# Kernel optimization log

Hardware: AMD Instinct MI355X
Metric: run time of the kernel (lower is better)

## Reference

```python
import jax, jax.numpy as jnp
import numpy as np

N_HEADS = 8
WINDOW = 7

def _conv1x1(x, W, b):
    # x: [B,H,W,C]; 1x1 conv == per-pixel matmul
    return jnp.einsum('bhwc,cd->bhwd', x, W) + b

def _to_heads(t, nh):
    # [B,H,W,C] -> channels-first reshape [B, nh, C//nh, H*W] (matches tf transpose+reshape)
    B, H, W, C = t.shape
    return jnp.transpose(t, (0, 3, 1, 2)).reshape(B, nh, C // nh, H * W)

def setup_inputs() -> dict:
    key = jax.random.key(0)
    ks = jax.random.split(key, 8)
    B, H, W, C = 2, 56, 56, 256
    x = jax.random.normal(ks[0], (B, H, W, C), dtype=jnp.float32)
    s = 1.0 / np.sqrt(C)
    Wq = jax.random.normal(ks[1], (C, C), dtype=jnp.float32) * s
    bq = jnp.zeros((C,), dtype=jnp.float32)
    Wk = jax.random.normal(ks[2], (C, C), dtype=jnp.float32) * s
    bk = jnp.zeros((C,), dtype=jnp.float32)
    Wv = jax.random.normal(ks[3], (C, C), dtype=jnp.float32) * s
    bv = jnp.zeros((C,), dtype=jnp.float32)
    # original initializes gamma to 0 (output == x); use small nonzero so the
    # attention path is observable in outputs/grads
    gamma = jax.random.normal(ks[4], (1,), dtype=jnp.float32) * 0.1
    return {"x": x, "Wq": Wq, "bq": bq, "Wk": Wk, "bk": bk, "Wv": Wv, "bv": bv, "gamma": gamma}

def reference(x, Wq, bq, Wk, bk, Wv, bv, gamma):
    B, H, W, C = x.shape
    p = WINDOW // 2
    xp = jnp.pad(x, ((0, 0), (p, p), (p, p), (0, 0)), mode='reflect')  # [B,Hp,Wp,C]
    q = _to_heads(_conv1x1(x, Wq, bq), N_HEADS)    # [B,nh,dk,HW]
    k = _to_heads(_conv1x1(xp, Wk, bk), N_HEADS)   # [B,nh,dk,HpWp]
    v = _to_heads(_conv1x1(xp, Wv, bv), N_HEADS)   # [B,nh,dk,HpWp]
    energy = jnp.einsum('bhdq,bhdk->bhqk', q, k)   # [B,nh,HW,HpWp]
    attn = jax.nn.softmax(energy, axis=-1)
    out = jnp.einsum('bhdk,bhqk->bhdq', v, attn)   # [B,nh,dk,HW]
    out = out.reshape(B, C, H, W).transpose(0, 2, 3, 1)
    return gamma * out + x
```

## Files before the change

### kernel.cpp

```cpp
#include <hip/hip_runtime.h>

typedef unsigned short u16;
typedef float f32x4 __attribute__((ext_vector_type(4)));
typedef short bf16x8 __attribute__((ext_vector_type(8)));

__device__ __forceinline__ u16 f2bf(float f) {
    unsigned u = __float_as_uint(f);
    u = (u + 0x7FFFu + ((u >> 16) & 1u)) >> 16;
    return (u16)u;
}

#define LOG2E 1.4426950408889634f

#if __has_builtin(__builtin_amdgcn_exp2f)
__device__ __forceinline__ float exp2_fast(float x) { return __builtin_amdgcn_exp2f(x); }
#else
__device__ __forceinline__ float exp2_fast(float x) { return __expf(x * 0.6931471805599453f); }
#endif

__device__ __forceinline__ unsigned pack2bf(float a, float b) {
    unsigned ua = __float_as_uint(a) + 0x8000u;
    unsigned ub = __float_as_uint(b) + 0x8000u;
#if __has_builtin(__builtin_amdgcn_perm)
    return __builtin_amdgcn_perm(ub, ua, 0x07060302u);
#else
    return ((ua >> 16) & 0xFFFFu) | (ub & 0xFFFF0000u);
#endif
}

#if __has_builtin(__builtin_amdgcn_cvt_pk_bf16_f32)
typedef __bf16 bf2_t __attribute__((ext_vector_type(2)));
__device__ __forceinline__ unsigned cvtpk(float a, float b) {
    bf2_t r = __builtin_amdgcn_cvt_pk_bf16_f32(a, b);
    return __builtin_bit_cast(unsigned, r);
}
#else
__device__ __forceinline__ unsigned cvtpk(float a, float b) { return pack2bf(a, b); }
#endif

__device__ __forceinline__ bf16x8 bc8(uint4 u) { return __builtin_bit_cast(bf16x8, u); }

#if __has_builtin(__builtin_amdgcn_global_load_lds)
typedef const __attribute__((address_space(1))) void* as1cv;
typedef __attribute__((address_space(3))) void* as3v;
__device__ __forceinline__ void dma16(const void* g, void* lds_base, int lane) {
    __builtin_amdgcn_global_load_lds((as1cv)g, (as3v)lds_base, 16, 0, 0);
}
#else
__device__ __forceinline__ void dma16(const void* g, void* lds_base, int lane) {
    *(uint4*)((char*)lds_base + lane * 16) = *(const uint4*)g;
}
#endif

#define BB 2
#define HH 56
#define SQ 3136
#define SKP 3200
#define VT_STRIDE 3200
#define CROWN 3584

#define WS_Q    0
#define WS_K    1605632
#define WS_VT   3211264
#define WS_WT   4849664
#define WS_CB   5046272

__global__ __launch_bounds__(256) void wprep_kernel(const float* __restrict__ Wq,
                                                    const float* __restrict__ Wk,
                                                    const float* __restrict__ Wv,
                                                    u16* __restrict__ wtf,
                                                    u16* __restrict__ vtb,
                                                    u16* __restrict__ crow) {
    __shared__ u16 T[64][68];
    int mode = blockIdx.z;
    const float* W = (mode == 0) ? Wq : ((mode == 1) ? Wk : Wv);
    float sc = (mode == 0) ? LOG2E : 1.0f;
    int kx = blockIdx.x * 64, dx = blockIdx.y * 64;
    int tid = threadIdx.x;
    int r16 = tid >> 4, c4 = (tid & 15) * 4;
#pragma unroll
    for (int p = 0; p < 4; ++p) {
        int kr = p * 16 + r16;
        float4 f = *(const float4*)&W[(size_t)(kx + kr) * 256 + dx + c4];
        T[kr][c4 + 0] = f2bf(f.x * sc);
        T[kr][c4 + 1] = f2bf(f.y * sc);
        T[kr][c4 + 2] = f2bf(f.z * sc);
        T[kr][c4 + 3] = f2bf(f.w * sc);
    }
    __syncthreads();
    int l16 = tid & 15, nt_loc = (tid >> 4) & 3, quad = (tid >> 6) & 3;
#pragma unroll
    for (int s_loc = 0; s_loc < 2; ++s_loc) {
        int k0 = s_loc * 32 + quad * 8;
        int d_loc = nt_loc * 16 + l16;
        u16 tmp[8];
#pragma unroll
        for (int j = 0; j < 8; ++j) tmp[j] = T[k0 + j][d_loc];
        int d = dx + d_loc;
        int nz = d >> 7, ntg = (d >> 4) & 7;
        int s = (kx >> 5) + s_loc;
        int f = (nz * 8 + s) * 8 + ntg;
        int L = quad * 16 + l16;
        *(uint4*)&wtf[(size_t)mode * 65536 + (size_t)f * 512 + (size_t)L * 8] = *(uint4*)tmp;
    }
    if (mode == 1 && kx == 0 && dx == 0) {
        for (int i = tid; i < CROWN; i += 256) {
            u16 v = 0;
            if (i < SQ) {
                int rr = i / 56, cc = i - rr * 56;
                int mr = (((rr >= 1) && (rr <= 3)) || ((rr >= 52) && (rr <= 54))) ? 2 : 1;
                int mc = (((cc >= 1) && (cc <= 3)) || ((cc >= 52) && (cc <= 54))) ? 2 : 1;
                int prod = mr * mc;
                v = (prod == 1) ? (u16)0x3F80 : ((prod == 2) ? (u16)0x4000 : (u16)0x4080);
            }
            crow[i] = v;
        }
    }
    if (mode == 2 && kx == 0 && dx == 0) {
        for (int i = tid; i < 512 * 8; i += 256) {
            int row = i >> 3, c16 = i & 7;
            *(uint4*)&vtb[(size_t)row * VT_STRIDE + SQ + c16 * 8] = (uint4){0, 0, 0, 0};
        }
    }
}

__global__ __launch_bounds__(256, 4) void proj_kernel(const float* __restrict__ x,
                                                      const u16* __restrict__ wtf,
                                                      const float* __restrict__ bq,
                                                      const float* __restrict__ bk,
                                                      const float* __restrict__ bv,
                                                      u16* __restrict__ qout,
                                                      u16* __restrict__ kout,
                                                      u16* __restrict__ vtout) {
    int mode = blockIdx.y, nz = blockIdx.z;
    int mbase = blockIdx.x * 64;
    int tid = threadIdx.x;
    int wave = tid >> 6, quad = (tid >> 4) & 3, l16 = tid & 15;
    const float* bias = (mode == 0) ? bq : ((mode == 1) ? bk : bv);
    float wsc = (mode == 0) ? LOG2E : 1.0f;
    const u16* wf = wtf + (size_t)mode * 65536 + (size_t)nz * 32768 + (size_t)(quad * 16 + l16) * 8;

    int m_a = mbase + wave * 16 + l16;
    const float* xr = x + (size_t)m_a * 256;

    f32x4 acc[8];
#pragma unroll
    for (int i = 0; i < 8; i++) acc[i] = (f32x4){0.f, 0.f, 0.f, 0.f};

#pragma unroll
    for (int s = 0; s < 8; ++s) {
        float4 f0 = *(const float4*)&xr[s * 32 + quad * 8];
        float4 f1 = *(const float4*)&xr[s * 32 + quad * 8 + 4];
        uint4 aw = (uint4){pack2bf(f0.x, f0.y), pack2bf(f0.z, f0.w),
                           pack2bf(f1.x, f1.y), pack2bf(f1.z, f1.w)};
        bf16x8 af = bc8(aw);
        if (mode == 2) {
#pragma unroll
            for (int nt = 0; nt < 8; nt++) {
                bf16x8 bfrag = *(const bf16x8*)&wf[(s * 8 + nt) * 512];
                acc[nt] = __builtin_amdgcn_mfma_f32_16x16x32_bf16(af, bfrag, acc[nt], 0, 0, 0);
            }
        } else {
#pragma unroll
            for (int nt = 0; nt < 8; nt++) {
                bf16x8 bfrag = *(const bf16x8*)&wf[(s * 8 + nt) * 512];
                acc[nt] = __builtin_amdgcn_mfma_f32_16x16x32_bf16(bfrag, af, acc[nt], 0, 0, 0);
            }
        }
    }

    if (mode == 2) {
        int mrow_base = mbase + wave * 16 + quad * 4;
        float mult[4];
#pragma unroll
        for (int p = 0; p < 4; ++p) {
            int m = mrow_base + p;
            int kp = (m >= SQ) ? m - SQ : m;
            int rr = kp / 56, cc = kp - rr * 56;
            float mr = (((rr >= 1) && (rr <= 3)) || ((rr >= 52) && (rr <= 54))) ? 2.f : 1.f;
            float mc = (((cc >= 1) && (cc <= 3)) || ((cc >= 52) && (cc <= 54))) ? 2.f : 1.f;
            mult[p] = mr * mc;
        }
#pragma unroll
        for (int nt = 0; nt < 8; nt++) {
            int c = nz * 128 + nt * 16 + l16;
            float bvv = bias[c];
#pragma unroll
            for (int p = 0; p < 4; p += 2) {
                int m = mrow_base + p;
                int bb = (m >= SQ) ? 1 : 0;
                int kp = m - bb * SQ;
                unsigned pk = pack2bf((acc[nt][p] + bvv) * mult[p],
                                      (acc[nt][p + 1] + bvv) * mult[p + 1]);
                *(unsigned*)&vtout[(size_t)(bb * 256 + c) * VT_STRIDE + kp] = pk;
            }
        }
    } else {
        u16* outp = (mode == 0) ? qout : kout;
#pragma unroll
        for (int nt = 0; nt < 8; nt++) {
            int c0 = nz * 128 + nt * 16 + quad * 4;
            float4 b4 = *(const float4*)&bias[c0];
            float v0 = acc[nt][0] + b4.x * wsc;
            float v1 = acc[nt][1] + b4.y * wsc;
            float v2 = acc[nt][2] + b4.z * wsc;
            float v3 = acc[nt][3] + b4.w * wsc;
            uint2 pk = (uint2){pack2bf(v0, v1), pack2bf(v2, v3)};
            *(uint2*)&outp[((size_t)m_a << 8) + c0] = pk;
        }
    }
}

__global__ __launch_bounds__(512, 6) void attn_kernel(const u16* __restrict__ qb,
                                                      const u16* __restrict__ kb,
                                                      const u16* __restrict__ vtb,
                                                      const u16* __restrict__ crow,
                                                      const float* __restrict__ x,
                                                      const float* __restrict__ gammap,
                                                      float* __restrict__ out) {
    __shared__ __align__(16) u16 S[19968];

    int tid = threadIdx.x;
    int w = tid >> 6, lane = tid & 63, quad = lane >> 4, l16 = lane & 15;
    int g = w & 3, qh = w >> 2;
    int bh = blockIdx.x;
    int b = bh >> 3, h = bh & 7;
    int qbase = b * SQ + blockIdx.y * 64 + qh * 32;

    bf16x8 qf[2];
#pragma unroll
    for (int i = 0; i < 2; ++i)
        qf[i] = *(const bf16x8*)&qb[((size_t)(qbase + i * 16 + l16) << 8) + h * 32 + quad * 8];

    const u16* kg = kb + ((size_t)(b * SQ) << 8) + h * 32;
    const u16* vg = vtb + (size_t)(b * 256 + h * 32) * VT_STRIDE;

    f32x4 o[2][2], lv[2];
#pragma unroll
    for (int i = 0; i < 2; ++i) {
        o[i][0] = (f32x4){0.f, 0.f, 0.f, 0.f};
        o[i][1] = (f32x4){0.f, 0.f, 0.f, 0.f};
        lv[i]   = (f32x4){0.f, 0.f, 0.f, 0.f};
    }

    auto stage = [&](int r_ch, int buf) {
        u16* base = &S[buf * 8192];
        int kbase = r_ch * 128;
        int grow = kbase + w * 16 + l16;
        if (grow > SQ - 1) grow = SQ - 1;
        dma16(kg + ((size_t)grow << 8) + (lane >> 4) * 8, base + w * 512, lane);
        int col = kbase + (2 * w + (lane >> 5)) * 8;
        dma16(vg + (size_t)(lane & 31) * VT_STRIDE + col, base + 4096 + w * 512, lane);
    };

    int tA = g, tB = g + 4;
    int vOffA = tA * 512 + (((quad >> 1) * 32 + l16) << 3) + (quad & 1) * 4;
    int vOffB = tB * 512 + (((quad >> 1) * 32 + l16) << 3) + (quad & 1) * 4;

    auto round_body = [&](int r, int bR) {
        const u16* Kl = &S[bR * 8192];
        const u16* Vl = Kl + 4096;
        const u16* cnt = &S[16384] + r * 128;
        f32x4 z = (f32x4){0.f, 0.f, 0.f, 0.f};

        float pA[2][4];
        {
            bf16x8 kfA = *(const bf16x8*)&Kl[tA * 512 + lane * 8];
            f32x4 eA0 = __builtin_amdgcn_mfma_f32_16x16x32_bf16(kfA, qf[0], z, 0, 0, 0);
            f32x4 eA1 = __builtin_amdgcn_mfma_f32_16x16x32_bf16(kfA, qf[1], z, 0, 0, 0);
#pragma unroll
            for (int j = 0; j < 4; ++j) pA[0][j] = exp2_fast(eA0[j]);
#pragma unroll
            for (int j = 0; j < 4; ++j) pA[1][j] = exp2_fast(eA1[j]);
        }
        float pB[2][4];
        {
            bf16x8 kfB = *(const bf16x8*)&Kl[tB * 512 + lane * 8];
            f32x4 eB0 = __builtin_amdgcn_mfma_f32_16x16x32_bf16(kfB, qf[0], z, 0, 0, 0);
            f32x4 eB1 = __builtin_amdgcn_mfma_f32_16x16x32_bf16(kfB, qf[1], z, 0, 0, 0);
#pragma unroll
            for (int j = 0; j < 4; ++j) pB[0][j] = exp2_fast(eB0[j]);
#pragma unroll
            for (int j = 0; j < 4; ++j) pB[1][j] = exp2_fast(eB1[j]);
        }
        uint2 ca = *(const uint2*)&cnt[tA * 16 + quad * 4];
        uint2 cc = *(const uint2*)&cnt[tB * 16 + quad * 4];
        bf16x8 cf = bc8((uint4){ca.x, ca.y, cc.x, cc.y});
        uint2 wA0 = *(const uint2*)&Vl[vOffA];
        uint2 wB0 = *(const uint2*)&Vl[vOffB];
        bf16x8 V0 = bc8((uint4){wA0.x, wA0.y, wB0.x, wB0.y});
        uint2 wA1 = *(const uint2*)&Vl[vOffA + 128];
        uint2 wB1 = *(const uint2*)&Vl[vOffB + 128];
        bf16x8 V1 = bc8((uint4){wA1.x, wA1.y, wB1.x, wB1.y});

#pragma unroll
        for (int i = 0; i < 2; ++i) {
            bf16x8 pa = bc8((uint4){cvtpk(pA[i][0], pA[i][1]), cvtpk(pA[i][2], pA[i][3]),
                                    cvtpk(pB[i][0], pB[i][1]), cvtpk(pB[i][2], pB[i][3])});
            o[i][0] = __builtin_amdgcn_mfma_f32_16x16x32_bf16(pa, V0, o[i][0], 0, 0, 0);
            o[i][1] = __builtin_amdgcn_mfma_f32_16x16x32_bf16(pa, V1, o[i][1], 0, 0, 0);
            lv[i]   = __builtin_amdgcn_mfma_f32_16x16x32_bf16(pa, cf, lv[i], 0, 0, 0);
        }
    };

    if (w < 7) dma16(crow + w * 512 + lane * 8, (char*)&S[16384] + w * 1024, lane);
    stage(0, 0);

    for (int r = 0; r < 25; ++r) {
        asm volatile("s_waitcnt vmcnt(0)" ::: "memory");
        __builtin_amdgcn_s_barrier();
        asm volatile("" ::: "memory");
        if (r + 1 < 25) stage(r + 1, (r + 1) & 1);
        round_body(r, r & 1);
    }
    __syncthreads();

    float* mg = (float*)&S[0];
    {
        int slot = ((qh * 2 + (g & 1)) * 64 + lane) * 24;
        if (g >= 2) {
            *(f32x4*)&mg[slot + 0]  = o[0][0];
            *(f32x4*)&mg[slot + 4]  = o[0][1];
            *(f32x4*)&mg[slot + 8]  = o[1][0];
            *(f32x4*)&mg[slot + 12] = o[1][1];
            *(f32x4*)&mg[slot + 16] = lv[0];
            *(f32x4*)&mg[slot + 20] = lv[1];
        }
        __syncthreads();
        if (g < 2) {
            o[0][0] += *(const f32x4*)&mg[slot + 0];
            o[0][1] += *(const f32x4*)&mg[slot + 4];
            o[1][0] += *(const f32x4*)&mg[slot + 8];
            o[1][1] += *(const f32x4*)&mg[slot + 12];
            lv[0]   += *(const f32x4*)&mg[slot + 16];
            lv[1]   += *(const f32x4*)&mg[slot + 20];
        }
        __syncthreads();
    }
    {
        int slot = (qh * 64 + lane) * 24;
        if (g == 1) {
            *(f32x4*)&mg[slot + 0]  = o[0][0];
            *(f32x4*)&mg[slot + 4]  = o[0][1];
            *(f32x4*)&mg[slot + 8]  = o[1][0];
            *(f32x4*)&mg[slot + 12] = o[1][1];
            *(f32x4*)&mg[slot + 16] = lv[0];
            *(f32x4*)&mg[slot + 20] = lv[1];
        }
        __syncthreads();
        if (g == 0) {
            o[0][0] += *(const f32x4*)&mg[slot + 0];
            o[0][1] += *(const f32x4*)&mg[slot + 4];
            o[1][0] += *(const f32x4*)&mg[slot + 8];
            o[1][1] += *(const f32x4*)&mg[slot + 12];
            lv[0]   += *(const f32x4*)&mg[slot + 16];
            lv[1]   += *(const f32x4*)&mg[slot + 20];
            float gam = gammap[0];
#pragma unroll
            for (int i = 0; i < 2; ++i) {
#pragma unroll
                for (int r2 = 0; r2 < 4; ++r2) {
                    float scl = gam / lv[i][r2];
                    int q = blockIdx.y * 64 + qh * 32 + i * 16 + quad * 4 + r2;
                    size_t base = ((size_t)(b * SQ + q) << 8) + h * 32 + l16;
                    out[base]      = o[i][0][r2] * scl + x[base];
                    out[base + 16] = o[i][1][r2] * scl + x[base + 16];
                }
            }
        }
    }
}

extern "C" void kernel_launch(void* const* d_in, const int* in_sizes, int n_in,
                              void* d_out, int out_size, void* d_ws, size_t ws_size,
                              hipStream_t stream) {
    const float* x     = (const float*)d_in[0];
    const float* Wq    = (const float*)d_in[1];
    const float* bq    = (const float*)d_in[2];
    const float* Wk    = (const float*)d_in[3];
    const float* bk    = (const float*)d_in[4];
    const float* Wv    = (const float*)d_in[5];
    const float* bv    = (const float*)d_in[6];
    const float* gamma = (const float*)d_in[7];
    float* out = (float*)d_out;

    u16* ws   = (u16*)d_ws;
    u16* qbuf = ws + WS_Q;
    u16* kbuf = ws + WS_K;
    u16* vtb  = ws + WS_VT;
    u16* wtf  = ws + WS_WT;
    u16* crow = ws + WS_CB;

    wprep_kernel<<<dim3(4, 4, 3), 256, 0, stream>>>(Wq, Wk, Wv, wtf, vtb, crow);
    proj_kernel<<<dim3(98, 3, 2), 256, 0, stream>>>(x, wtf, bq, bk, bv, qbuf, kbuf, vtb);
    attn_kernel<<<dim3(16, 49), 512, 0, stream>>>(qbuf, kbuf, vtb, crow, x, gamma, out);
}
```

Baseline: 153.1 us.

## Store Q/K/V and bf16 x in MFMA-fragment-tiled layout for contiguous DMA

Adds an xprep kernel that converts x to bf16 once, pre-arranged in MFMA fragment order, so proj_kernel no longer converts it three times per tile. The projection outputs for Q, K and V are written in 16-row tiles laid out exactly as the attention kernel's LDS fragments expect. Each K/V staging DMA becomes one contiguous 1 KB read instead of strided row gathers, and the row clamp is dropped in favour of zero-padded tail tiles. The cost is an extra kernel launch and an extra pass over x, plus scattered small stores in the projection epilogue.

```diff
diff --git a/kernel.cpp b/kernel.cpp
--- a/kernel.cpp
+++ b/kernel.cpp
@@ -55,21 +55,42 @@
 #define BB 2
 #define HH 56
 #define SQ 3136
-#define SKP 3200
-#define VT_STRIDE 3200
 #define CROWN 3584
 
 #define WS_Q    0
 #define WS_K    1605632
-#define WS_VT   3211264
-#define WS_WT   4849664
-#define WS_CB   5046272
+#define WS_V    3244032
+#define WS_WT   4882432
+#define WS_CB   5079040
+#define WS_XB   5082624
+
+__global__ __launch_bounds__(256) void xprep_kernel(const float* __restrict__ x,
+                                                    u16* __restrict__ xbf) {
+    __shared__ float T[16][256];
+    int tile = blockIdx.x, tid = threadIdx.x;
+    int r = tid >> 4, c0 = (tid & 15) * 16;
+    const float* src = x + ((size_t)tile * 16 + r) * 256 + c0;
+#pragma unroll
+    for (int k = 0; k < 4; ++k)
+        *(float4*)&T[r][c0 + k * 4] = *(const float4*)&src[k * 4];
+    __syncthreads();
+#pragma unroll
+    for (int e = 0; e < 2; ++e) {
+        int g = tid + e * 256;
+        int s = g >> 6, L = g & 63;
+        const float* row = &T[L & 15][s * 32 + (L >> 4) * 8];
+        uint4 pk = (uint4){pack2bf(row[0], row[1]), pack2bf(row[2], row[3]),
+                           pack2bf(row[4], row[5]), pack2bf(row[6], row[7])};
+        *(uint4*)&xbf[(size_t)tile * 4096 + (size_t)g * 8] = pk;
+    }
+}
 
 __global__ __launch_bounds__(256) void wprep_kernel(const float* __restrict__ Wq,
                                                     const float* __restrict__ Wk,
                                                     const float* __restrict__ Wv,
                                                     u16* __restrict__ wtf,
-                                                    u16* __restrict__ vtb,
+                                                    u16* __restrict__ kbf,
+                                                    u16* __restrict__ vbf,
                                                     u16* __restrict__ crow) {
     __shared__ u16 T[64][68];
     int mode = blockIdx.z;
@@ -102,6 +123,14 @@
         int f = (nz * 8 + s) * 8 + ntg;
         int L = quad * 16 + l16;
         *(uint4*)&wtf[(size_t)mode * 65536 + (size_t)f * 512 + (size_t)L * 8] = *(uint4*)tmp;
+    }
+    uint4 z4 = (uint4){0, 0, 0, 0};
+    if (mode == 0 && kx == 0 && dx == 0) {
+        for (int i = tid; i < 4096; i += 256) {
+            int bb = i >> 11, rem = i & 2047;
+            int t = 196 + (rem >> 9), off = (rem & 511) * 8;
+            *(uint4*)&kbf[(((size_t)(bb * 200 + t)) << 12) + off] = z4;
+        }
     }
     if (mode == 1 && kx == 0 && dx == 0) {
         for (int i = tid; i < CROWN; i += 256) {
@@ -117,31 +146,30 @@
         }
     }
     if (mode == 2 && kx == 0 && dx == 0) {
-        for (int i = tid; i < 512 * 8; i += 256) {
-            int row = i >> 3, c16 = i & 7;
-            *(uint4*)&vtb[(size_t)row * VT_STRIDE + SQ + c16 * 8] = (uint4){0, 0, 0, 0};
-        }
-    }
-}
-
-__global__ __launch_bounds__(256, 4) void proj_kernel(const float* __restrict__ x,
+        for (int i = tid; i < 4096; i += 256) {
+            int bh = i >> 8, rem = i & 255;
+            int rgp = 196 + (rem >> 6), off = (rem & 63) * 8;
+            *(uint4*)&vbf[(((size_t)(bh * 200 + rgp)) << 9) + off] = z4;
+        }
+    }
+}
+
+__global__ __launch_bounds__(256, 4) void proj_kernel(const u16* __restrict__ xbf,
                                                       const u16* __restrict__ wtf,
                                                       const float* __restrict__ bq,
                                                       const float* __restrict__ bk,
                                                       const float* __restrict__ bv,
-                                                      u16* __restrict__ qout,
-                                                      u16* __restrict__ kout,
-                                                      u16* __restrict__ vtout) {
+                                                      u16* __restrict__ qbf,
+                                                      u16* __restrict__ kbf,
+                                                      u16* __restrict__ vbf) {
     int mode = blockIdx.y, nz = blockIdx.z;
     int mbase = blockIdx.x * 64;
     int tid = threadIdx.x;
-    int wave = tid >> 6, quad = (tid >> 4) & 3, l16 = tid & 15;
+    int wave = tid >> 6, lane = tid & 63, quad = (tid >> 4) & 3, l16 = tid & 15;
     const float* bias = (mode == 0) ? bq : ((mode == 1) ? bk : bv);
     float wsc = (mode == 0) ? LOG2E : 1.0f;
-    const u16* wf = wtf + (size_t)mode * 65536 + (size_t)nz * 32768 + (size_t)(quad * 16 + l16) * 8;
-
-    int m_a = mbase + wave * 16 + l16;
-    const float* xr = x + (size_t)m_a * 256;
+    const u16* wf = wtf + (size_t)mode * 65536 + (size_t)nz * 32768 + (size_t)lane * 8;
+    const u16* xt = xbf + (((size_t)(mbase >> 4) + wave) << 12);
 
     f32x4 acc[8];
 #pragma unroll
@@ -149,11 +177,7 @@
 
 #pragma unroll
     for (int s = 0; s < 8; ++s) {
-        float4 f0 = *(const float4*)&xr[s * 32 + quad * 8];
-        float4 f1 = *(const float4*)&xr[s * 32 + quad * 8 + 4];
-        uint4 aw = (uint4){pack2bf(f0.x, f0.y), pack2bf(f0.z, f0.w),
-                           pack2bf(f1.x, f1.y), pack2bf(f1.z, f1.w)};
-        bf16x8 af = bc8(aw);
+        bf16x8 af = *(const bf16x8*)&xt[(s << 9) + lane * 8];
         if (mode == 2) {
 #pragma unroll
             for (int nt = 0; nt < 8; nt++) {
@@ -170,12 +194,13 @@
     }
 
     if (mode == 2) {
-        int mrow_base = mbase + wave * 16 + quad * 4;
+        int b_ = (mbase >= SQ) ? 1 : 0;
+        int kp0 = mbase - b_ * SQ + wave * 16 + quad * 4;
+        int rg = (mbase - b_ * SQ + wave * 16) >> 4;
         float mult[4];
 #pragma unroll
         for (int p = 0; p < 4; ++p) {
-            int m = mrow_base + p;
-            int kp = (m >= SQ) ? m - SQ : m;
+            int kp = kp0 + p;
             int rr = kp / 56, cc = kp - rr * 56;
             float mr = (((rr >= 1) && (rr <= 3)) || ((rr >= 52) && (rr <= 54))) ? 2.f : 1.f;
             float mc = (((cc >= 1) && (cc <= 3)) || ((cc >= 52) && (cc <= 54))) ? 2.f : 1.f;
@@ -185,18 +210,19 @@
         for (int nt = 0; nt < 8; nt++) {
             int c = nz * 128 + nt * 16 + l16;
             float bvv = bias[c];
-#pragma unroll
-            for (int p = 0; p < 4; p += 2) {
-                int m = mrow_base + p;
-                int bb = (m >= SQ) ? 1 : 0;
-                int kp = m - bb * SQ;
-                unsigned pk = pack2bf((acc[nt][p] + bvv) * mult[p],
-                                      (acc[nt][p + 1] + bvv) * mult[p + 1]);
-                *(unsigned*)&vtout[(size_t)(bb * 256 + c) * VT_STRIDE + kp] = pk;
-            }
+            int h_idx = nz * 4 + (nt >> 1);
+            int L = (nt & 1) * 16 + l16 + ((quad >> 1) & 1) * 32;
+            float va0 = (acc[nt][0] + bvv) * mult[0];
+            float va1 = (acc[nt][1] + bvv) * mult[1];
+            float va2 = (acc[nt][2] + bvv) * mult[2];
+            float va3 = (acc[nt][3] + bvv) * mult[3];
+            uint2 pk = (uint2){pack2bf(va0, va1), pack2bf(va2, va3)};
+            *(uint2*)&vbf[(((size_t)((b_ * 8 + h_idx) * 200 + rg)) << 9) + L * 8 + (quad & 1) * 4] = pk;
         }
     } else {
-        u16* outp = (mode == 0) ? qout : kout;
+        u16* outp = (mode == 0) ? qbf : kbf;
+        int t = (mbase >> 4) + wave;
+        int tt = (mode == 0) ? t : (t + (t >= 196 ? 4 : 0));
 #pragma unroll
         for (int nt = 0; nt < 8; nt++) {
             int c0 = nz * 128 + nt * 16 + quad * 4;
@@ -205,8 +231,10 @@
             float v1 = acc[nt][1] + b4.y * wsc;
             float v2 = acc[nt][2] + b4.z * wsc;
             float v3 = acc[nt][3] + b4.w * wsc;
+            int s_idx = nz * 4 + (nt >> 1);
+            int Lrow = ((nt & 1) * 2 + (quad >> 1)) * 16 + l16;
             uint2 pk = (uint2){pack2bf(v0, v1), pack2bf(v2, v3)};
-            *(uint2*)&outp[((size_t)m_a << 8) + c0] = pk;
+            *(uint2*)&outp[(((size_t)(tt * 8 + s_idx)) << 9) + Lrow * 8 + (quad & 1) * 4] = pk;
         }
     }
 }
@@ -225,15 +253,15 @@
     int g = w & 3, qh = w >> 2;
     int bh = blockIdx.x;
     int b = bh >> 3, h = bh & 7;
-    int qbase = b * SQ + blockIdx.y * 64 + qh * 32;
-
+
+    int qtile = b * 196 + blockIdx.y * 4 + qh * 2;
     bf16x8 qf[2];
 #pragma unroll
     for (int i = 0; i < 2; ++i)
-        qf[i] = *(const bf16x8*)&qb[((size_t)(qbase + i * 16 + l16) << 8) + h * 32 + quad * 8];
-
-    const u16* kg = kb + ((size_t)(b * SQ) << 8) + h * 32;
-    const u16* vg = vtb + (size_t)(b * 256 + h * 32) * VT_STRIDE;
+        qf[i] = *(const bf16x8*)&qb[(((size_t)(qtile + i) * 8 + h) << 9) + lane * 8];
+
+    const u16* kg = kb + ((size_t)(b * 200) << 12);
+    const u16* vg = vtb + (((size_t)((b * 8 + h) * 200)) << 9);
 
     f32x4 o[2][2], lv[2];
 #pragma unroll
@@ -245,12 +273,9 @@
 
     auto stage = [&](int r_ch, int buf) {
         u16* base = &S[buf * 8192];
-        int kbase = r_ch * 128;
-        int grow = kbase + w * 16 + l16;
-        if (grow > SQ - 1) grow = SQ - 1;
-        dma16(kg + ((size_t)grow << 8) + (lane >> 4) * 8, base + w * 512, lane);
-        int col = kbase + (2 * w + (lane >> 5)) * 8;
-        dma16(vg + (size_t)(lane & 31) * VT_STRIDE + col, base + 4096 + w * 512, lane);
+        int rg = r_ch * 8 + w;
+        dma16(kg + (((size_t)rg * 8 + h) << 9) + lane * 8, base + w * 512, lane);
+        dma16(vg + (((size_t)rg) << 9) + lane * 8, base + 4096 + w * 512, lane);
     };
 
     int tA = g, tB = g + 4;
@@ -385,13 +410,15 @@
     float* out = (float*)d_out;
 
     u16* ws   = (u16*)d_ws;
-    u16* qbuf = ws + WS_Q;
-    u16* kbuf = ws + WS_K;
-    u16* vtb  = ws + WS_VT;
+    u16* qbf  = ws + WS_Q;
+    u16* kbf  = ws + WS_K;
+    u16* vbf  = ws + WS_V;
     u16* wtf  = ws + WS_WT;
     u16* crow = ws + WS_CB;
-
-    wprep_kernel<<<dim3(4, 4, 3), 256, 0, stream>>>(Wq, Wk, Wv, wtf, vtb, crow);
-    proj_kernel<<<dim3(98, 3, 2), 256, 0, stream>>>(x, wtf, bq, bk, bv, qbuf, kbuf, vtb);
-    attn_kernel<<<dim3(16, 49), 512, 0, stream>>>(qbuf, kbuf, vtb, crow, x, gamma, out);
-}
+    u16* xbf  = ws + WS_XB;
+
+    xprep_kernel<<<392, 256, 0, stream>>>(x, xbf);
+    wprep_kernel<<<dim3(4, 4, 3), 256, 0, stream>>>(Wq, Wk, Wv, wtf, kbf, vbf, crow);
+    proj_kernel<<<dim3(98, 3, 2), 256, 0, stream>>>(xbf, wtf, bq, bk, bv, qbf, kbf, vbf);
+    attn_kernel<<<dim3(16, 49), 512, 0, stream>>>(qbf, kbf, vbf, crow, x, gamma, out);
+}
```

New measurement: 134.8 us. 12.0% less time.
